# Performance work log

Measured on AMD Instinct MI355X. Metric: run time of the kernel, lower is better.

The kernel has to match this reference:

```python
import jax, jax.numpy as jnp
import numpy as np

N_NODES = 131072
N_EDGES = 4194304
H1, H2 = 16, 1


def setup_inputs() -> dict:
    key = jax.random.key(0)
    k = jax.random.split(key, 6)
    x = jax.random.uniform(k[0], (N_NODES, 2), dtype=jnp.float32)
    edge_index = jax.random.randint(k[1], (2, N_EDGES), 0, N_NODES, dtype=jnp.int64)
    # GCNConv weights (glorot-ish scale) and zero biases
    W1 = jax.random.normal(k[2], (2, H1), dtype=jnp.float32) * 0.5
    b1 = jnp.zeros((H1,), dtype=jnp.float32)
    W2 = jax.random.normal(k[3], (H1, H2), dtype=jnp.float32) * 0.25
    b2 = jnp.zeros((H2,), dtype=jnp.float32)
    return {"x": x, "W1": W1, "b1": b1, "W2": W2, "b2": b2, "edge_index": edge_index}


def gcn_layer(x, W, b, src, dst, n):
    # PyG GCNConv: h = D^{-1/2} (A+I) D^{-1/2} (x W) + b  (self-loops already in src/dst)
    h = x @ W                                              # [N, F_out]
    deg = jax.ops.segment_sum(jnp.ones(dst.shape[0], h.dtype), dst, num_segments=n)
    dinv = jax.lax.rsqrt(deg)                              # deg >= 1 thanks to self-loops
    norm = dinv[src] * dinv[dst]                           # [E+N]
    out = jax.ops.segment_sum(h[src] * norm[:, None], dst, num_segments=n)
    return out + b


def reference(x, W1, b1, W2, b2, edge_index):
    n = x.shape[0]
    loops = jnp.arange(n, dtype=edge_index.dtype)
    src = jnp.concatenate([edge_index[0], loops])          # add self-loops once
    dst = jnp.concatenate([edge_index[1], loops])
    h = jax.nn.relu(gcn_layer(x, W1, b1, src, dst, n))
    h = gcn_layer(h, W2, b2, src, dst, n)                  # [N, 1]
    scores = jax.nn.sigmoid(h)
    return scores[edge_index[0]]                           # gather per-edge source score [E, 1]
```

## Files before the change

kernel.cpp:

```cpp
#include <hip/hip_runtime.h>
#include <cmath>

typedef unsigned int uint;

constexpr int N  = 131072;
constexpr int E  = 4194304;
constexpr int F  = 16;
constexpr int NB = 512;
constexpr int NBLK  = 512;
constexpr int SCT   = 512;
constexpr int CHUNK = 8192;
constexpr int EPT   = 16;
constexpr int NSCAN = NB * NBLK;
constexpr int CAP   = 10240;
constexpr int SLOTS = CAP / SCT;
constexpr int LPN   = 8;

__global__ void __launch_bounds__(SCT) k_hist(const int* __restrict__ dst,
                                              uint* __restrict__ hist_blocks) {
    __shared__ uint hw[8 * NB];
    int t = threadIdx.x, g = blockIdx.x;
    int w = t >> 6;
#pragma unroll
    for (int k = 0; k < 8; ++k) hw[k * SCT + t] = 0;
    __syncthreads();
    int base = g * CHUNK;
#pragma unroll
    for (int k = 0; k < EPT; ++k)
        atomicAdd(&hw[w * NB + (dst[base + k * SCT + t] >> 8)], 1u);
    __syncthreads();
    uint sum = 0;
#pragma unroll
    for (int k = 0; k < 8; ++k) sum += hw[k * NB + t];
    hist_blocks[(size_t)t * NBLK + g] = sum;
}

__global__ void k_scan_up(const uint* __restrict__ hist, uint* __restrict__ bsum) {
    __shared__ uint s[256];
    int g = blockIdx.x, t = threadIdx.x;
    s[t] = hist[(size_t)g * 256 + t];
    __syncthreads();
    for (int off = 128; off > 0; off >>= 1) {
        if (t < off) s[t] += s[t + off];
        __syncthreads();
    }
    if (t == 0) bsum[g] = s[0];
}

__global__ void k_scan_mid(uint* bsum) {
    __shared__ uint s[256];
    int t = threadIdx.x;
    uint v[4]; uint sum = 0;
#pragma unroll
    for (int k = 0; k < 4; ++k) { v[k] = bsum[t * 4 + k]; sum += v[k]; }
    s[t] = sum;
    __syncthreads();
    for (int off = 1; off < 256; off <<= 1) {
        uint x = (t >= off) ? s[t - off] : 0u;
        __syncthreads();
        s[t] += x;
        __syncthreads();
    }
    uint base = (t == 0) ? 0u : s[t - 1];
#pragma unroll
    for (int k = 0; k < 4; ++k) { uint old = v[k]; bsum[t * 4 + k] = base; base += old; }
}

__global__ void k_scan_down(const uint* __restrict__ hist, const uint* __restrict__ bsum,
                            uint* __restrict__ scanned) {
    __shared__ uint s[256];
    int g = blockIdx.x, t = threadIdx.x;
    uint v = hist[(size_t)g * 256 + t];
    s[t] = v;
    __syncthreads();
    for (int off = 1; off < 256; off <<= 1) {
        uint x = (t >= off) ? s[t - off] : 0u;
        __syncthreads();
        s[t] += x;
        __syncthreads();
    }
    scanned[(size_t)g * 256 + t] = bsum[g] + s[t] - v;
}

__global__ void __launch_bounds__(SCT) k_scatter(
        const int* __restrict__ src, const int* __restrict__ dst,
        const uint* __restrict__ scanned, uint* __restrict__ part) {
    __shared__ uint h[NB];
    __shared__ uint wb[NB];
    __shared__ uint wsum[8];
    __shared__ uint vals[CHUNK];
    __shared__ uint addr[CHUNK];
    int t = threadIdx.x, g = blockIdx.x;
    int lane = t & 63, w = t >> 6;
    h[t] = 0;
    __syncthreads();
    int d[EPT], s[EPT];
    int base = g * CHUNK;
#pragma unroll
    for (int k = 0; k < EPT; ++k) {
        int e = base + k * SCT + t;
        d[k] = dst[e];
        s[k] = src[e];
        atomicAdd(&h[d[k] >> 8], 1u);
    }
    __syncthreads();
    uint v = h[t];
    uint sv = v;
#pragma unroll
    for (int off = 1; off < 64; off <<= 1) {
        uint n = __shfl_up(sv, off);
        if (lane >= off) sv += n;
    }
    if (lane == 63) wsum[w] = sv;
    __syncthreads();
    uint wo = 0;
    for (int i = 0; i < w; ++i) wo += wsum[i];
    sv += wo;
    uint ex = sv - v;
    wb[t] = scanned[(size_t)t * NBLK + g] - ex;
    h[t] = ex;
    __syncthreads();
#pragma unroll
    for (int k = 0; k < EPT; ++k) {
        int b = d[k] >> 8;
        uint slot = atomicAdd(&h[b], 1u);
        vals[slot] = ((uint)s[k] << 8) | (uint)(d[k] & 255);
        addr[slot] = wb[b] + slot;
    }
    __syncthreads();
#pragma unroll
    for (int k = 0; k < EPT; ++k) {
        int i = k * SCT + t;
        part[addr[i]] = vals[i];
    }
}

__global__ void __launch_bounds__(SCT) k_sort(
        uint* part, const uint* __restrict__ scanned,
        const float* __restrict__ x,
        uint* __restrict__ csr, float* __restrict__ dinv, float2* __restrict__ y) {
    __shared__ uint hw[8 * 256];
    __shared__ uint cnt[256];
    __shared__ uint sc[256];
    __shared__ uint wsum[4];
    __shared__ uint srt[CAP];
    int t = threadIdx.x, b = blockIdx.x;
    int lane = t & 63, w = t >> 6;
#pragma unroll
    for (int k = 0; k < 4; ++k) hw[k * SCT + t] = 0;
    __syncthreads();
    uint S0 = scanned[(size_t)b * NBLK];
    uint S1 = (b == NB - 1) ? (uint)E : scanned[(size_t)(b + 1) * NBLK];
    uint pk[SLOTS];
#pragma unroll
    for (int k = 0; k < SLOTS; ++k) {
        uint i = S0 + (uint)(k * SCT + t);
        pk[k] = (i < S1) ? part[i] : 0xFFFFFFFFu;
        if (pk[k] != 0xFFFFFFFFu) atomicAdd(&hw[w * 256 + (pk[k] & 255u)], 1u);
    }
    __syncthreads();
    if (t < 256) {
        uint tot = 0;
#pragma unroll
        for (int k = 0; k < 8; ++k) {
            uint c = hw[k * 256 + t];
            hw[k * 256 + t] = tot;
            tot += c;
        }
        cnt[t] = tot;
        uint sv = tot;
#pragma unroll
        for (int off = 1; off < 64; off <<= 1) {
            uint n = __shfl_up(sv, off);
            if (lane >= off) sv += n;
        }
        if (lane == 63) wsum[t >> 6] = sv;
        sc[t] = sv;
    }
    __syncthreads();
    if (t < 256) {
        uint wo = 0;
        for (int i = 0; i < (t >> 6); ++i) wo += wsum[i];
        sc[t] += wo;
    }
    __syncthreads();
#pragma unroll
    for (int k = 0; k < SLOTS; ++k) {
        if (pk[k] != 0xFFFFFFFFu) {
            uint bin = pk[k] & 255u;
            uint slot = (sc[bin] - cnt[bin]) + atomicAdd(&hw[w * 256 + bin], 1u);
            srt[slot] = pk[k] >> 8;
        }
    }
    __syncthreads();
    uint L = S1 - S0;
    for (uint i = t; i < L; i += SCT) part[S0 + i] = srt[i];
    if (t < 256) {
        int node = (b << 8) + t;
        csr[node] = S0 + (sc[t] - cnt[t]);
        float di = rsqrtf(1.0f + (float)cnt[t]);
        dinv[node] = di;
        float2 xv = ((const float2*)x)[node];
        y[node] = make_float2(di * xv.x, di * xv.y);
    }
}

__global__ void k_l1(const uint* __restrict__ srcs, const uint* __restrict__ csr,
                     const float2* __restrict__ y, const float* __restrict__ dinv,
                     const float* __restrict__ W1, const float* __restrict__ b1,
                     const float* __restrict__ W2, float* __restrict__ g2) {
    int tid = blockIdx.x * blockDim.x + threadIdx.x;
    int node = tid >> 3, lane = tid & (LPN - 1);
    uint o0 = csr[node];
    uint o1 = (node == N - 1) ? (uint)E : csr[node + 1];
    float A0 = 0.0f, A1 = 0.0f;
    for (uint j = o0 + lane; j < o1; j += LPN) {
        float2 ys = y[srcs[j]];
        A0 += ys.x; A1 += ys.y;
    }
    A0 += __shfl_xor(A0, 1); A0 += __shfl_xor(A0, 2); A0 += __shfl_xor(A0, 4);
    A1 += __shfl_xor(A1, 1); A1 += __shfl_xor(A1, 2); A1 += __shfl_xor(A1, 4);
    float di = dinv[node];
    float2 yn = y[node];
    A0 = di * (A0 + yn.x);
    A1 = di * (A1 + yn.y);
    float acc = 0.0f;
#pragma unroll
    for (int f = lane; f < F; f += LPN) {
        float v = fmaf(A0, W1[f], fmaf(A1, W1[F + f], b1[f]));
        acc = fmaf(fmaxf(v, 0.0f), W2[f], acc);
    }
    acc += __shfl_xor(acc, 1); acc += __shfl_xor(acc, 2); acc += __shfl_xor(acc, 4);
    if (lane == 0) g2[node] = di * acc;
}

__global__ void k_l2(const uint* __restrict__ srcs, const uint* __restrict__ csr,
                     const float* __restrict__ g2, const float* __restrict__ dinv,
                     const float* __restrict__ b2, float* __restrict__ scores) {
    int tid = blockIdx.x * blockDim.x + threadIdx.x;
    int node = tid >> 3, lane = tid & (LPN - 1);
    uint o0 = csr[node];
    uint o1 = (node == N - 1) ? (uint)E : csr[node + 1];
    float acc = 0.0f;
    for (uint j = o0 + lane; j < o1; j += LPN) acc += g2[srcs[j]];
    acc += __shfl_xor(acc, 1); acc += __shfl_xor(acc, 2); acc += __shfl_xor(acc, 4);
    if (lane == 0) {
        float v = fmaf(dinv[node], acc + g2[node], b2[0]);
        scores[node] = 1.0f / (1.0f + expf(-v));
    }
}

__global__ void k_out(const int* __restrict__ src, const float* __restrict__ scores,
                      float* __restrict__ out) {
    int e = blockIdx.x * blockDim.x + threadIdx.x;
    if (e < E) out[e] = scores[src[e]];
}

extern "C" void kernel_launch(void* const* d_in, const int* in_sizes, int n_in,
                              void* d_out, int out_size, void* d_ws, size_t ws_size,
                              hipStream_t stream) {
    const float* x  = (const float*)d_in[0];
    const float* W1 = (const float*)d_in[1];
    const float* b1 = (const float*)d_in[2];
    const float* W2 = (const float*)d_in[3];
    const float* b2 = (const float*)d_in[4];
    const int*   ei = (const int*)d_in[5];
    const int* src = ei;
    const int* dst = ei + E;

    uint* hist_blocks = (uint*)d_ws;
    uint* scanned     = hist_blocks + NSCAN;
    uint* bsum        = scanned + NSCAN;
    uint* csr         = bsum + 1024;
    float* dinv       = (float*)(csr + N + 2);
    float2* y         = (float2*)(dinv + N);
    float* g2         = (float*)(y + N);
    float* scores     = g2 + N;

    uint* part  = (uint*)d_out;
    float* out  = (float*)d_out;

    k_hist     <<<NBLK,          SCT, 0, stream>>>(dst, hist_blocks);
    k_scan_up  <<<NSCAN / 256,   256, 0, stream>>>(hist_blocks, bsum);
    k_scan_mid <<<1,             256, 0, stream>>>(bsum);
    k_scan_down<<<NSCAN / 256,   256, 0, stream>>>(hist_blocks, bsum, scanned);
    k_scatter  <<<NBLK,          SCT, 0, stream>>>(src, dst, scanned, part);
    k_sort     <<<NB,            SCT, 0, stream>>>(part, scanned, x, csr, dinv, y);
    k_l1       <<<(N * LPN) / 256, 256, 0, stream>>>(part, csr, y, dinv, W1, b1, W2, g2);
    k_l2       <<<(N * LPN) / 256, 256, 0, stream>>>(part, csr, g2, dinv, b2, scores);
    k_out      <<<E / 256,       256, 0, stream>>>(src, scores, out);
}
```

Before: 191.3 us.

## Vectorize edge loads, fold scan-mid into scan-down, use 16 lanes per node

The histogram, scatter and output-gather kernels now read edge indices as int4, and k_out writes float4, so fewer and wider memory transactions are issued. The single-block k_scan_mid launch is removed. Each k_scan_down block instead reduces the block sums that precede it, which adds redundant work per block but saves one serialized launch. The aggregation kernels move from 8 to 16 lanes per node, giving one hidden feature per lane in layer 1 and fewer loop trips per lane, at the cost of more threads and an extra shuffle stage.

```diff
diff --git a/kernel.cpp b/kernel.cpp
--- a/kernel.cpp
+++ b/kernel.cpp
@@ -14,7 +14,7 @@
 constexpr int NSCAN = NB * NBLK;
 constexpr int CAP   = 10240;
 constexpr int SLOTS = CAP / SCT;
-constexpr int LPN   = 8;
+constexpr int LPN   = 16;
 
 __global__ void __launch_bounds__(SCT) k_hist(const int* __restrict__ dst,
                                               uint* __restrict__ hist_blocks) {
@@ -24,10 +24,16 @@
 #pragma unroll
     for (int k = 0; k < 8; ++k) hw[k * SCT + t] = 0;
     __syncthreads();
-    int base = g * CHUNK;
-#pragma unroll
-    for (int k = 0; k < EPT; ++k)
-        atomicAdd(&hw[w * NB + (dst[base + k * SCT + t] >> 8)], 1u);
+    const int4* dst4 = (const int4*)dst;
+    int base4 = g * (CHUNK / 4);
+#pragma unroll
+    for (int k = 0; k < EPT / 4; ++k) {
+        int4 d4 = dst4[base4 + k * SCT + t];
+        atomicAdd(&hw[w * NB + (d4.x >> 8)], 1u);
+        atomicAdd(&hw[w * NB + (d4.y >> 8)], 1u);
+        atomicAdd(&hw[w * NB + (d4.z >> 8)], 1u);
+        atomicAdd(&hw[w * NB + (d4.w >> 8)], 1u);
+    }
     __syncthreads();
     uint sum = 0;
 #pragma unroll
@@ -47,13 +53,22 @@
     if (t == 0) bsum[g] = s[0];
 }
 
-__global__ void k_scan_mid(uint* bsum) {
+__global__ void k_scan_down(const uint* __restrict__ hist, const uint* __restrict__ bsum,
+                            uint* __restrict__ scanned) {
+    __shared__ uint red[256];
     __shared__ uint s[256];
-    int t = threadIdx.x;
-    uint v[4]; uint sum = 0;
-#pragma unroll
-    for (int k = 0; k < 4; ++k) { v[k] = bsum[t * 4 + k]; sum += v[k]; }
-    s[t] = sum;
+    int g = blockIdx.x, t = threadIdx.x;
+    uint p = 0;
+    for (int i = t; i < g; i += 256) p += bsum[i];
+    red[t] = p;
+    __syncthreads();
+    for (int off = 128; off > 0; off >>= 1) {
+        if (t < off) red[t] += red[t + off];
+        __syncthreads();
+    }
+    uint base = red[0];
+    uint v = hist[(size_t)g * 256 + t];
+    s[t] = v;
     __syncthreads();
     for (int off = 1; off < 256; off <<= 1) {
         uint x = (t >= off) ? s[t - off] : 0u;
@@ -61,25 +76,7 @@
         s[t] += x;
         __syncthreads();
     }
-    uint base = (t == 0) ? 0u : s[t - 1];
-#pragma unroll
-    for (int k = 0; k < 4; ++k) { uint old = v[k]; bsum[t * 4 + k] = base; base += old; }
-}
-
-__global__ void k_scan_down(const uint* __restrict__ hist, const uint* __restrict__ bsum,
-                            uint* __restrict__ scanned) {
-    __shared__ uint s[256];
-    int g = blockIdx.x, t = threadIdx.x;
-    uint v = hist[(size_t)g * 256 + t];
-    s[t] = v;
-    __syncthreads();
-    for (int off = 1; off < 256; off <<= 1) {
-        uint x = (t >= off) ? s[t - off] : 0u;
-        __syncthreads();
-        s[t] += x;
-        __syncthreads();
-    }
-    scanned[(size_t)g * 256 + t] = bsum[g] + s[t] - v;
+    scanned[(size_t)g * 256 + t] = base + s[t] - v;
 }
 
 __global__ void __launch_bounds__(SCT) k_scatter(
@@ -95,13 +92,19 @@
     h[t] = 0;
     __syncthreads();
     int d[EPT], s[EPT];
-    int base = g * CHUNK;
-#pragma unroll
-    for (int k = 0; k < EPT; ++k) {
-        int e = base + k * SCT + t;
-        d[k] = dst[e];
-        s[k] = src[e];
-        atomicAdd(&h[d[k] >> 8], 1u);
+    const int4* src4 = (const int4*)src;
+    const int4* dst4 = (const int4*)dst;
+    int base4 = g * (CHUNK / 4);
+#pragma unroll
+    for (int k = 0; k < EPT / 4; ++k) {
+        int4 d4 = dst4[base4 + k * SCT + t];
+        int4 s4 = src4[base4 + k * SCT + t];
+        d[4 * k + 0] = d4.x; d[4 * k + 1] = d4.y; d[4 * k + 2] = d4.z; d[4 * k + 3] = d4.w;
+        s[4 * k + 0] = s4.x; s[4 * k + 1] = s4.y; s[4 * k + 2] = s4.z; s[4 * k + 3] = s4.w;
+        atomicAdd(&h[d4.x >> 8], 1u);
+        atomicAdd(&h[d4.y >> 8], 1u);
+        atomicAdd(&h[d4.z >> 8], 1u);
+        atomicAdd(&h[d4.w >> 8], 1u);
     }
     __syncthreads();
     uint v = h[t];
@@ -210,7 +213,7 @@
                      const float* __restrict__ W1, const float* __restrict__ b1,
                      const float* __restrict__ W2, float* __restrict__ g2) {
     int tid = blockIdx.x * blockDim.x + threadIdx.x;
-    int node = tid >> 3, lane = tid & (LPN - 1);
+    int node = tid >> 4, lane = tid & (LPN - 1);
     uint o0 = csr[node];
     uint o1 = (node == N - 1) ? (uint)E : csr[node + 1];
     float A0 = 0.0f, A1 = 0.0f;
@@ -218,19 +221,19 @@
         float2 ys = y[srcs[j]];
         A0 += ys.x; A1 += ys.y;
     }
-    A0 += __shfl_xor(A0, 1); A0 += __shfl_xor(A0, 2); A0 += __shfl_xor(A0, 4);
-    A1 += __shfl_xor(A1, 1); A1 += __shfl_xor(A1, 2); A1 += __shfl_xor(A1, 4);
+    A0 += __shfl_xor(A0, 1); A0 += __shfl_xor(A0, 2);
+    A0 += __shfl_xor(A0, 4); A0 += __shfl_xor(A0, 8);
+    A1 += __shfl_xor(A1, 1); A1 += __shfl_xor(A1, 2);
+    A1 += __shfl_xor(A1, 4); A1 += __shfl_xor(A1, 8);
     float di = dinv[node];
     float2 yn = y[node];
     A0 = di * (A0 + yn.x);
     A1 = di * (A1 + yn.y);
-    float acc = 0.0f;
-#pragma unroll
-    for (int f = lane; f < F; f += LPN) {
-        float v = fmaf(A0, W1[f], fmaf(A1, W1[F + f], b1[f]));
-        acc = fmaf(fmaxf(v, 0.0f), W2[f], acc);
-    }
-    acc += __shfl_xor(acc, 1); acc += __shfl_xor(acc, 2); acc += __shfl_xor(acc, 4);
+    int f = lane;
+    float v = fmaf(A0, W1[f], fmaf(A1, W1[F + f], b1[f]));
+    float acc = fmaxf(v, 0.0f) * W2[f];
+    acc += __shfl_xor(acc, 1); acc += __shfl_xor(acc, 2);
+    acc += __shfl_xor(acc, 4); acc += __shfl_xor(acc, 8);
     if (lane == 0) g2[node] = di * acc;
 }
 
@@ -238,12 +241,13 @@
                      const float* __restrict__ g2, const float* __restrict__ dinv,
                      const float* __restrict__ b2, float* __restrict__ scores) {
     int tid = blockIdx.x * blockDim.x + threadIdx.x;
-    int node = tid >> 3, lane = tid & (LPN - 1);
+    int node = tid >> 4, lane = tid & (LPN - 1);
     uint o0 = csr[node];
     uint o1 = (node == N - 1) ? (uint)E : csr[node + 1];
     float acc = 0.0f;
     for (uint j = o0 + lane; j < o1; j += LPN) acc += g2[srcs[j]];
-    acc += __shfl_xor(acc, 1); acc += __shfl_xor(acc, 2); acc += __shfl_xor(acc, 4);
+    acc += __shfl_xor(acc, 1); acc += __shfl_xor(acc, 2);
+    acc += __shfl_xor(acc, 4); acc += __shfl_xor(acc, 8);
     if (lane == 0) {
         float v = fmaf(dinv[node], acc + g2[node], b2[0]);
         scores[node] = 1.0f / (1.0f + expf(-v));
@@ -252,8 +256,15 @@
 
 __global__ void k_out(const int* __restrict__ src, const float* __restrict__ scores,
                       float* __restrict__ out) {
-    int e = blockIdx.x * blockDim.x + threadIdx.x;
-    if (e < E) out[e] = scores[src[e]];
+    int i = blockIdx.x * blockDim.x + threadIdx.x;
+    if (i >= E / 4) return;
+    int4 s4 = ((const int4*)src)[i];
+    float4 o;
+    o.x = scores[s4.x];
+    o.y = scores[s4.y];
+    o.z = scores[s4.z];
+    o.w = scores[s4.w];
+    ((float4*)out)[i] = o;
 }
 
 extern "C" void kernel_launch(void* const* d_in, const int* in_sizes, int n_in,
@@ -282,11 +293,10 @@
 
     k_hist     <<<NBLK,          SCT, 0, stream>>>(dst, hist_blocks);
     k_scan_up  <<<NSCAN / 256,   256, 0, stream>>>(hist_blocks, bsum);
-    k_scan_mid <<<1,             256, 0, stream>>>(bsum);
     k_scan_down<<<NSCAN / 256,   256, 0, stream>>>(hist_blocks, bsum, scanned);
     k_scatter  <<<NBLK,          SCT, 0, stream>>>(src, dst, scanned, part);
     k_sort     <<<NB,            SCT, 0, stream>>>(part, scanned, x, csr, dinv, y);
     k_l1       <<<(N * LPN) / 256, 256, 0, stream>>>(part, csr, y, dinv, W1, b1, W2, g2);
     k_l2       <<<(N * LPN) / 256, 256, 0, stream>>>(part, csr, g2, dinv, b2, scores);
-    k_out      <<<E / 256,       256, 0, stream>>>(src, scores, out);
-}
+    k_out      <<<E / 4 / 256,   256, 0, stream>>>(src, scores, out);
+}
```

Result: no change. 190.4 us (-0.5%).
